# Kernel tuning notes

Measured on AMD Instinct MI355X. Metric: run time of the kernel, lower is better.

Reference implementation:

```python
import jax, jax.numpy as jnp
import numpy as np

EPS = 1e-07


def setup_inputs() -> dict:
    key = jax.random.key(0)
    k1, k2, k3, k4, k5, k6 = jax.random.split(key, 6)
    B, S, E = 128, 512, 64  # batch, seq_len == n_items, emb_size
    user_emb = jax.random.normal(k1, (B, S, E), dtype=jnp.float32)
    item_emb = jax.random.normal(k2, (B, S, E), dtype=jnp.float32)
    cluster_weights = jax.random.uniform(k3, (B, S, 1), dtype=jnp.float32)
    # binary keep-mask over sequence positions (multiplicative)
    last_item_mask = (jax.random.uniform(k4, (B, 1, S)) > 0.5).astype(jnp.float32)
    proj_w = jax.random.normal(k5, (1, 1), dtype=jnp.float32)
    proj_b = jax.random.normal(k6, (1,), dtype=jnp.float32)
    return {
        "user_emb": user_emb,
        "item_emb": item_emb,
        "cluster_weights": cluster_weights,
        "last_item_mask": last_item_mask,
        "proj_w": proj_w,
        "proj_b": proj_b,
    }


def reference(user_emb, item_emb, cluster_weights, last_item_mask, proj_w, proj_b):
    # L2-normalize with clamped norm (matches torch.clamp(norm, 1e-7))
    u = user_emb / jnp.maximum(jnp.linalg.norm(user_emb, axis=-1, keepdims=True), EPS)
    v = item_emb / jnp.maximum(jnp.linalg.norm(item_emb, axis=-1, keepdims=True), EPS)
    # cosine sim: [B, n_items, seq_len] (n_items == seq_len == S)
    cos = jnp.einsum("bse,bne->bns", u, v)
    # cluster_weights [B,S,1] broadcasts over the seq_len axis, indexed by dim1
    # (faithful to torch broadcast of [B,N,S,1] * [B,S,1,1] with N == S)
    sims = cos * cluster_weights  # [B,N,S]
    # Linear(1,1) + sigmoid applied elementwise (scalar affine)
    sims = jax.nn.sigmoid(sims * proj_w[0, 0] + proj_b[0])
    # permute to [B, seq_len, n_items], mask [B,1,S] broadcasts over last axis
    sims = jnp.swapaxes(sims, 1, 2) * last_item_mask
    # max over dim 2 -> [B, seq_len]
    return jnp.max(sims, axis=2)
```

## Files before the change

kernel.cpp:

```cpp
#include <hip/hip_runtime.h>
#include <hip/hip_bf16.h>
#include <math.h>

#define B_ 128
#define S_ 512
#define E_ 64
#define PAD_ 72

typedef short bf16x8 __attribute__((ext_vector_type(8)));
typedef float f32x4 __attribute__((ext_vector_type(4)));

__device__ __forceinline__ unsigned short f2b(float f) {
  __hip_bfloat16 h = __float2bfloat16(f);
  unsigned short u;
  __builtin_memcpy(&u, &h, 2);
  return u;
}

__device__ __forceinline__ void norm_store(const f32x4 x[4], float scl_num,
                                           unsigned short* dst) {
  float ss = 0.f;
#pragma unroll
  for (int i = 0; i < 4; ++i)
#pragma unroll
    for (int j = 0; j < 4; ++j) ss = fmaf(x[i][j], x[i][j], ss);
  ss += __shfl_xor(ss, 16);
  ss += __shfl_xor(ss, 32);
  float s = scl_num / fmaxf(sqrtf(ss), 1e-7f);
  bf16x8 o0, o1;
#pragma unroll
  for (int i = 0; i < 2; ++i)
#pragma unroll
    for (int j = 0; j < 4; ++j) {
      o0[i * 4 + j] = (short)f2b(x[i][j] * s);
      o1[i * 4 + j] = (short)f2b(x[i + 2][j] * s);
    }
  *(bf16x8*)dst = o0;
  *(bf16x8*)(dst + 8) = o1;
}

__global__ __launch_bounds__(1024) void fused_kernel(
    const float* __restrict__ ue, const float* __restrict__ ve,
    const float* __restrict__ cw, const float* __restrict__ mask,
    const float* __restrict__ pw, const float* __restrict__ pb,
    float* __restrict__ out) {
  __shared__ unsigned short vlds[S_ * PAD_];
  __shared__ unsigned short ulds[256 * PAD_];
  __shared__ float comb[4][256];

  const int bx = blockIdx.x;
  const int b = (bx & 7) * 16 + (bx >> 4);
  const int shalf = (bx >> 3) & 1;

  const int tid = threadIdx.x;
  const int wv = tid >> 6;
  const int lane = tid & 63;
  const int c = lane & 15;
  const int g = lane >> 4;
  const int ws = wv >> 2;
  const int wn = wv & 3;

  const float w0 = pw[0];
  const float* __restrict__ vb = ve + (size_t)b * S_ * E_;
  const float* __restrict__ cwb = cw + (size_t)b * S_;
  const float* __restrict__ ub = ue + ((size_t)b * S_ + shalf * 256) * E_;
  const float* __restrict__ mb = mask + (size_t)b * S_;

  const int vr0 = wv * 32 + c, vr1 = vr0 + 16, ur = wv * 16 + c;
  const f32x4* pv0 = (const f32x4*)(vb + (size_t)vr0 * E_ + g * 16);
  const f32x4* pv1 = (const f32x4*)(vb + (size_t)vr1 * E_ + g * 16);
  const f32x4* pu = (const f32x4*)(ub + (size_t)ur * E_ + g * 16);
  f32x4 xv0[4], xv1[4], xu[4];
#pragma unroll
  for (int i = 0; i < 4; ++i) {
    xv0[i] = pv0[i];
    xv1[i] = pv1[i];
    xu[i] = pu[i];
  }
  float cw0 = cwb[vr0] * w0;
  float cw1 = cwb[vr1] * w0;
  float pen[8];
#pragma unroll
  for (int j = 0; j < 8; ++j)
    pen[j] = (mb[(wn * 8 + j) * 16 + c] > 0.5f) ? 0.0f : -1e30f;

  norm_store(xv0, cw0, vlds + (size_t)vr0 * PAD_ + g * 16);
  norm_store(xv1, cw1, vlds + (size_t)vr1 * PAD_ + g * 16);
  norm_store(xu, 1.0f, ulds + (size_t)ur * PAD_ + g * 16);

  __syncthreads();

  const unsigned short* urp = ulds + (size_t)(ws * 64 + c) * PAD_ + g * 8;
  bf16x8 a[4][2];
#pragma unroll
  for (int st = 0; st < 4; ++st) {
    a[st][0] = *(const bf16x8*)(urp + st * 16 * PAD_);
    a[st][1] = *(const bf16x8*)(urp + st * 16 * PAD_ + 32);
  }

  float r[4][4];
#pragma unroll
  for (int st = 0; st < 4; ++st)
#pragma unroll
    for (int i = 0; i < 4; ++i) r[st][i] = -INFINITY;

#pragma unroll
  for (int j = 0; j < 8; ++j) {
    int it = wn * 8 + j;
    const unsigned short* vr = vlds + (size_t)(it * 16 + c) * PAD_ + g * 8;
    bf16x8 b0 = *(const bf16x8*)(vr);
    bf16x8 b1 = *(const bf16x8*)(vr + 32);
    f32x4 ci = {pen[j], pen[j], pen[j], pen[j]};
#pragma unroll
    for (int st = 0; st < 4; ++st) {
      f32x4 acc = __builtin_amdgcn_mfma_f32_16x16x32_bf16(a[st][0], b0, ci, 0, 0, 0);
      acc = __builtin_amdgcn_mfma_f32_16x16x32_bf16(a[st][1], b1, acc, 0, 0, 0);
      r[st][0] = fmaxf(r[st][0], acc[0]);
      r[st][1] = fmaxf(r[st][1], acc[1]);
      r[st][2] = fmaxf(r[st][2], acc[2]);
      r[st][3] = fmaxf(r[st][3], acc[3]);
    }
  }

#pragma unroll
  for (int st = 0; st < 4; ++st)
#pragma unroll
    for (int i = 0; i < 4; ++i) {
      float v = r[st][i];
      v = fmaxf(v, __shfl_xor(v, 1)); v = fmaxf(v, __shfl_xor(v, 2));
      v = fmaxf(v, __shfl_xor(v, 4)); v = fmaxf(v, __shfl_xor(v, 8));
      r[st][i] = v;
    }

  if (c == 0) {
#pragma unroll
    for (int st = 0; st < 4; ++st)
#pragma unroll
      for (int i = 0; i < 4; ++i)
        comb[wn][ws * 64 + st * 16 + g * 4 + i] = r[st][i];
  }

  __syncthreads();

  if (tid < 256) {
    float v = fmaxf(fmaxf(comb[0][tid], comb[1][tid]),
                    fmaxf(comb[2][tid], comb[3][tid]));
    float bias = pb[0];
    out[(size_t)b * S_ + shalf * 256 + tid] =
        (v < -1e29f) ? 0.0f : 1.0f / (1.0f + expf(-(v + bias)));
  }
}

extern "C" void kernel_launch(void* const* d_in, const int* in_sizes, int n_in,
                              void* d_out, int out_size, void* d_ws, size_t ws_size,
                              hipStream_t stream) {
  const float* ue = (const float*)d_in[0];
  const float* ve = (const float*)d_in[1];
  const float* cw = (const float*)d_in[2];
  const float* mask = (const float*)d_in[3];
  const float* pw = (const float*)d_in[4];
  const float* pb = (const float*)d_in[5];
  float* out = (float*)d_out;

  hipLaunchKernelGGL(fused_kernel, dim3(2 * B_), dim3(1024), 0, stream,
                     ue, ve, cw, mask, pw, pb, out);
}
```

Before: 19.13 us.

## Split each batch across four 512-thread blocks and normalize user rows in registers

The grid changes from 256 blocks of 1024 threads, each covering half of a batch's rows, to 512 blocks of 512 threads, each covering a quarter. User-embedding rows are now loaded in the layout the MFMA A operand needs, then normalized and converted to bf16 directly in registers, which removes the user LDS buffer and one round trip through shared memory. The aim is more resident blocks and better latency hiding, helped by launch bounds of 4 blocks per CU. The cost is that each batch's item embeddings are now normalized four times instead of twice, which adds global reads and redundant normalize work.

Result: slower. 27.90 us (+45.8%).

```diff
diff --git a/kernel.cpp b/kernel.cpp
--- a/kernel.cpp
+++ b/kernel.cpp
@@ -17,40 +17,17 @@
   return u;
 }
 
-__device__ __forceinline__ void norm_store(const f32x4 x[4], float scl_num,
-                                           unsigned short* dst) {
-  float ss = 0.f;
-#pragma unroll
-  for (int i = 0; i < 4; ++i)
-#pragma unroll
-    for (int j = 0; j < 4; ++j) ss = fmaf(x[i][j], x[i][j], ss);
-  ss += __shfl_xor(ss, 16);
-  ss += __shfl_xor(ss, 32);
-  float s = scl_num / fmaxf(sqrtf(ss), 1e-7f);
-  bf16x8 o0, o1;
-#pragma unroll
-  for (int i = 0; i < 2; ++i)
-#pragma unroll
-    for (int j = 0; j < 4; ++j) {
-      o0[i * 4 + j] = (short)f2b(x[i][j] * s);
-      o1[i * 4 + j] = (short)f2b(x[i + 2][j] * s);
-    }
-  *(bf16x8*)dst = o0;
-  *(bf16x8*)(dst + 8) = o1;
-}
-
-__global__ __launch_bounds__(1024) void fused_kernel(
+__global__ __launch_bounds__(512, 4) void fused_kernel(
     const float* __restrict__ ue, const float* __restrict__ ve,
     const float* __restrict__ cw, const float* __restrict__ mask,
     const float* __restrict__ pw, const float* __restrict__ pb,
     float* __restrict__ out) {
   __shared__ unsigned short vlds[S_ * PAD_];
-  __shared__ unsigned short ulds[256 * PAD_];
-  __shared__ float comb[4][256];
+  __shared__ float comb[4][128];
 
   const int bx = blockIdx.x;
-  const int b = (bx & 7) * 16 + (bx >> 4);
-  const int shalf = (bx >> 3) & 1;
+  const int b = (bx & 7) * 16 + (bx >> 5);
+  const int sq = (bx >> 3) & 3;
 
   const int tid = threadIdx.x;
   const int wv = tid >> 6;
@@ -63,40 +40,70 @@
   const float w0 = pw[0];
   const float* __restrict__ vb = ve + (size_t)b * S_ * E_;
   const float* __restrict__ cwb = cw + (size_t)b * S_;
-  const float* __restrict__ ub = ue + ((size_t)b * S_ + shalf * 256) * E_;
+  const float* __restrict__ ub = ue + ((size_t)b * S_ + sq * 128) * E_;
   const float* __restrict__ mb = mask + (size_t)b * S_;
 
-  const int vr0 = wv * 32 + c, vr1 = vr0 + 16, ur = wv * 16 + c;
-  const f32x4* pv0 = (const f32x4*)(vb + (size_t)vr0 * E_ + g * 16);
-  const f32x4* pv1 = (const f32x4*)(vb + (size_t)vr1 * E_ + g * 16);
-  const f32x4* pu = (const f32x4*)(ub + (size_t)ur * E_ + g * 16);
-  f32x4 xv0[4], xv1[4], xu[4];
+  f32x4 xu[4][4];
 #pragma unroll
-  for (int i = 0; i < 4; ++i) {
-    xv0[i] = pv0[i];
-    xv1[i] = pv1[i];
-    xu[i] = pu[i];
+  for (int st = 0; st < 4; ++st) {
+    const float* r = ub + (size_t)(ws * 64 + st * 16 + c) * E_;
+    xu[st][0] = *(const f32x4*)(r + 8 * g);
+    xu[st][1] = *(const f32x4*)(r + 8 * g + 4);
+    xu[st][2] = *(const f32x4*)(r + 8 * g + 32);
+    xu[st][3] = *(const f32x4*)(r + 8 * g + 36);
   }
-  float cw0 = cwb[vr0] * w0;
-  float cw1 = cwb[vr1] * w0;
   float pen[8];
 #pragma unroll
   for (int j = 0; j < 8; ++j)
     pen[j] = (mb[(wn * 8 + j) * 16 + c] > 0.5f) ? 0.0f : -1e30f;
 
-  norm_store(xv0, cw0, vlds + (size_t)vr0 * PAD_ + g * 16);
-  norm_store(xv1, cw1, vlds + (size_t)vr1 * PAD_ + g * 16);
-  norm_store(xu, 1.0f, ulds + (size_t)ur * PAD_ + g * 16);
+#pragma unroll
+  for (int q = 0; q < 4; ++q) {
+    const int row = wv * 64 + q * 16 + c;
+    const float* r = vb + (size_t)row * E_ + g * 16;
+    f32x4 x0 = *(const f32x4*)(r);
+    f32x4 x1 = *(const f32x4*)(r + 4);
+    f32x4 x2 = *(const f32x4*)(r + 8);
+    f32x4 x3 = *(const f32x4*)(r + 12);
+    float ss = 0.f;
+#pragma unroll
+    for (int j = 0; j < 4; ++j)
+      ss = fmaf(x0[j], x0[j], fmaf(x1[j], x1[j], fmaf(x2[j], x2[j], fmaf(x3[j], x3[j], ss))));
+    ss += __shfl_xor(ss, 16);
+    ss += __shfl_xor(ss, 32);
+    float s = (w0 * cwb[row]) / fmaxf(sqrtf(ss), 1e-7f);
+    bf16x8 o0, o1;
+#pragma unroll
+    for (int j = 0; j < 4; ++j) {
+      o0[j] = (short)f2b(x0[j] * s); o0[4 + j] = (short)f2b(x1[j] * s);
+      o1[j] = (short)f2b(x2[j] * s); o1[4 + j] = (short)f2b(x3[j] * s);
+    }
+    unsigned short* dst = vlds + (size_t)row * PAD_ + g * 16;
+    *(bf16x8*)dst = o0;
+    *(bf16x8*)(dst + 8) = o1;
+  }
 
-  __syncthreads();
-
-  const unsigned short* urp = ulds + (size_t)(ws * 64 + c) * PAD_ + g * 8;
   bf16x8 a[4][2];
 #pragma unroll
   for (int st = 0; st < 4; ++st) {
-    a[st][0] = *(const bf16x8*)(urp + st * 16 * PAD_);
-    a[st][1] = *(const bf16x8*)(urp + st * 16 * PAD_ + 32);
+    float ss = 0.f;
+#pragma unroll
+    for (int i = 0; i < 4; ++i)
+#pragma unroll
+      for (int j = 0; j < 4; ++j) ss = fmaf(xu[st][i][j], xu[st][i][j], ss);
+    ss += __shfl_xor(ss, 16);
+    ss += __shfl_xor(ss, 32);
+    float s = 1.0f / fmaxf(sqrtf(ss), 1e-7f);
+#pragma unroll
+    for (int j = 0; j < 4; ++j) {
+      a[st][0][j] = (short)f2b(xu[st][0][j] * s);
+      a[st][0][4 + j] = (short)f2b(xu[st][1][j] * s);
+      a[st][1][j] = (short)f2b(xu[st][2][j] * s);
+      a[st][1][4 + j] = (short)f2b(xu[st][3][j] * s);
+    }
   }
+
+  __syncthreads();
 
   float r[4][4];
 #pragma unroll
@@ -106,7 +113,7 @@
 
 #pragma unroll
   for (int j = 0; j < 8; ++j) {
-    int it = wn * 8 + j;
+    const int it = wn * 8 + j;
     const unsigned short* vr = vlds + (size_t)(it * 16 + c) * PAD_ + g * 8;
     bf16x8 b0 = *(const bf16x8*)(vr);
     bf16x8 b1 = *(const bf16x8*)(vr + 32);
@@ -142,11 +149,11 @@
 
   __syncthreads();
 
-  if (tid < 256) {
+  if (tid < 128) {
     float v = fmaxf(fmaxf(comb[0][tid], comb[1][tid]),
                     fmaxf(comb[2][tid], comb[3][tid]));
     float bias = pb[0];
-    out[(size_t)b * S_ + shalf * 256 + tid] =
+    out[(size_t)b * S_ + sq * 128 + tid] =
         (v < -1e29f) ? 0.0f : 1.0f / (1.0f + expf(-(v + bias)));
   }
 }
@@ -162,6 +169,6 @@
   const float* pb = (const float*)d_in[5];
   float* out = (float*)d_out;
 
-  hipLaunchKernelGGL(fused_kernel, dim3(2 * B_), dim3(1024), 0, stream,
+  hipLaunchKernelGGL(fused_kernel, dim3(4 * B_), dim3(512), 0, stream,
                      ue, ve, cw, mask, pw, pb, out);
 }
```

## Split item-embedding staging into two phases to overlap loads with MFMA

Applied to the files above, without the earlier changes.

The item embeddings are now staged in two halves. Each block first loads and normalizes the half matching its own user rows and runs MFMAs on it. The load of the other half is issued before that compute, and that half is normalized and stored after it, separated by an extra barrier. The aim is to hide part of the global load latency behind matrix work, at the cost of one more __syncthreads and holding the second half's registers live during the first compute phase.

Result: faster. 18.39 us (-3.9%).

```diff
diff --git a/kernel.cpp b/kernel.cpp
--- a/kernel.cpp
+++ b/kernel.cpp
@@ -15,28 +15,6 @@
   unsigned short u;
   __builtin_memcpy(&u, &h, 2);
   return u;
-}
-
-__device__ __forceinline__ void norm_store(const f32x4 x[4], float scl_num,
-                                           unsigned short* dst) {
-  float ss = 0.f;
-#pragma unroll
-  for (int i = 0; i < 4; ++i)
-#pragma unroll
-    for (int j = 0; j < 4; ++j) ss = fmaf(x[i][j], x[i][j], ss);
-  ss += __shfl_xor(ss, 16);
-  ss += __shfl_xor(ss, 32);
-  float s = scl_num / fmaxf(sqrtf(ss), 1e-7f);
-  bf16x8 o0, o1;
-#pragma unroll
-  for (int i = 0; i < 2; ++i)
-#pragma unroll
-    for (int j = 0; j < 4; ++j) {
-      o0[i * 4 + j] = (short)f2b(x[i][j] * s);
-      o1[i * 4 + j] = (short)f2b(x[i + 2][j] * s);
-    }
-  *(bf16x8*)dst = o0;
-  *(bf16x8*)(dst + 8) = o1;
 }
 
 __global__ __launch_bounds__(1024) void fused_kernel(
@@ -66,29 +44,72 @@
   const float* __restrict__ ub = ue + ((size_t)b * S_ + shalf * 256) * E_;
   const float* __restrict__ mb = mask + (size_t)b * S_;
 
-  const int vr0 = wv * 32 + c, vr1 = vr0 + 16, ur = wv * 16 + c;
-  const f32x4* pv0 = (const f32x4*)(vb + (size_t)vr0 * E_ + g * 16);
-  const f32x4* pv1 = (const f32x4*)(vb + (size_t)vr1 * E_ + g * 16);
-  const f32x4* pu = (const f32x4*)(ub + (size_t)ur * E_ + g * 16);
-  f32x4 xv0[4], xv1[4], xu[4];
-#pragma unroll
-  for (int i = 0; i < 4; ++i) {
-    xv0[i] = pv0[i];
-    xv1[i] = pv1[i];
-    xu[i] = pu[i];
-  }
-  float cw0 = cwb[vr0] * w0;
-  float cw1 = cwb[vr1] * w0;
+  const int vrow_own = shalf * 256 + wv * 16 + c;
+  const int vrow_oth = (1 - shalf) * 256 + wv * 16 + c;
+  const int urow = wv * 16 + c;
+
+  const float* pv = vb + (size_t)vrow_own * E_ + g * 16;
+  const float* pu = ub + (size_t)urow * E_ + g * 16;
+  f32x4 xv[4], xu[4];
+#pragma unroll
+  for (int i = 0; i < 4; ++i) xv[i] = ((const f32x4*)pv)[i];
+#pragma unroll
+  for (int i = 0; i < 4; ++i) xu[i] = ((const f32x4*)pu)[i];
+  float cwv = cwb[vrow_own];
   float pen[8];
 #pragma unroll
-  for (int j = 0; j < 8; ++j)
-    pen[j] = (mb[(wn * 8 + j) * 16 + c] > 0.5f) ? 0.0f : -1e30f;
-
-  norm_store(xv0, cw0, vlds + (size_t)vr0 * PAD_ + g * 16);
-  norm_store(xv1, cw1, vlds + (size_t)vr1 * PAD_ + g * 16);
-  norm_store(xu, 1.0f, ulds + (size_t)ur * PAD_ + g * 16);
+  for (int j = 0; j < 4; ++j) {
+    pen[j] = (mb[(shalf * 16 + wn * 4 + j) * 16 + c] > 0.5f) ? 0.0f : -1e30f;
+    pen[4 + j] =
+        (mb[((1 - shalf) * 16 + wn * 4 + j) * 16 + c] > 0.5f) ? 0.0f : -1e30f;
+  }
+
+  {
+    float ss = 0.f;
+#pragma unroll
+    for (int i = 0; i < 4; ++i)
+#pragma unroll
+      for (int j = 0; j < 4; ++j) ss = fmaf(xv[i][j], xv[i][j], ss);
+    ss += __shfl_xor(ss, 16);
+    ss += __shfl_xor(ss, 32);
+    float s = (w0 * cwv) / fmaxf(sqrtf(ss), 1e-7f);
+    bf16x8 o0, o1;
+#pragma unroll
+    for (int j = 0; j < 4; ++j) {
+      o0[j] = (short)f2b(xv[0][j] * s); o0[4 + j] = (short)f2b(xv[1][j] * s);
+      o1[j] = (short)f2b(xv[2][j] * s); o1[4 + j] = (short)f2b(xv[3][j] * s);
+    }
+    unsigned short* dst = vlds + (size_t)vrow_own * PAD_ + g * 16;
+    *(bf16x8*)dst = o0;
+    *(bf16x8*)(dst + 8) = o1;
+  }
+  {
+    float ss = 0.f;
+#pragma unroll
+    for (int i = 0; i < 4; ++i)
+#pragma unroll
+      for (int j = 0; j < 4; ++j) ss = fmaf(xu[i][j], xu[i][j], ss);
+    ss += __shfl_xor(ss, 16);
+    ss += __shfl_xor(ss, 32);
+    float s = 1.0f / fmaxf(sqrtf(ss), 1e-7f);
+    bf16x8 o0, o1;
+#pragma unroll
+    for (int j = 0; j < 4; ++j) {
+      o0[j] = (short)f2b(xu[0][j] * s); o0[4 + j] = (short)f2b(xu[1][j] * s);
+      o1[j] = (short)f2b(xu[2][j] * s); o1[4 + j] = (short)f2b(xu[3][j] * s);
+    }
+    unsigned short* dst = ulds + (size_t)urow * PAD_ + g * 16;
+    *(bf16x8*)dst = o0;
+    *(bf16x8*)(dst + 8) = o1;
+  }
 
   __syncthreads();
+
+  const float* py = vb + (size_t)vrow_oth * E_ + g * 16;
+  f32x4 yv[4];
+#pragma unroll
+  for (int i = 0; i < 4; ++i) yv[i] = ((const f32x4*)py)[i];
+  float cwo = cwb[vrow_oth];
 
   const unsigned short* urp = ulds + (size_t)(ws * 64 + c) * PAD_ + g * 8;
   bf16x8 a[4][2];
@@ -105,12 +126,52 @@
     for (int i = 0; i < 4; ++i) r[st][i] = -INFINITY;
 
 #pragma unroll
-  for (int j = 0; j < 8; ++j) {
-    int it = wn * 8 + j;
+  for (int j = 0; j < 4; ++j) {
+    const int it = shalf * 16 + wn * 4 + j;
     const unsigned short* vr = vlds + (size_t)(it * 16 + c) * PAD_ + g * 8;
     bf16x8 b0 = *(const bf16x8*)(vr);
     bf16x8 b1 = *(const bf16x8*)(vr + 32);
     f32x4 ci = {pen[j], pen[j], pen[j], pen[j]};
+#pragma unroll
+    for (int st = 0; st < 4; ++st) {
+      f32x4 acc = __builtin_amdgcn_mfma_f32_16x16x32_bf16(a[st][0], b0, ci, 0, 0, 0);
+      acc = __builtin_amdgcn_mfma_f32_16x16x32_bf16(a[st][1], b1, acc, 0, 0, 0);
+      r[st][0] = fmaxf(r[st][0], acc[0]);
+      r[st][1] = fmaxf(r[st][1], acc[1]);
+      r[st][2] = fmaxf(r[st][2], acc[2]);
+      r[st][3] = fmaxf(r[st][3], acc[3]);
+    }
+  }
+
+  {
+    float ss = 0.f;
+#pragma unroll
+    for (int i = 0; i < 4; ++i)
+#pragma unroll
+      for (int j = 0; j < 4; ++j) ss = fmaf(yv[i][j], yv[i][j], ss);
+    ss += __shfl_xor(ss, 16);
+    ss += __shfl_xor(ss, 32);
+    float s = (w0 * cwo) / fmaxf(sqrtf(ss), 1e-7f);
+    bf16x8 o0, o1;
+#pragma unroll
+    for (int j = 0; j < 4; ++j) {
+      o0[j] = (short)f2b(yv[0][j] * s); o0[4 + j] = (short)f2b(yv[1][j] * s);
+      o1[j] = (short)f2b(yv[2][j] * s); o1[4 + j] = (short)f2b(yv[3][j] * s);
+    }
+    unsigned short* dst = vlds + (size_t)vrow_oth * PAD_ + g * 16;
+    *(bf16x8*)dst = o0;
+    *(bf16x8*)(dst + 8) = o1;
+  }
+
+  __syncthreads();
+
+#pragma unroll
+  for (int j = 0; j < 4; ++j) {
+    const int it = (1 - shalf) * 16 + wn * 4 + j;
+    const unsigned short* vr = vlds + (size_t)(it * 16 + c) * PAD_ + g * 8;
+    bf16x8 b0 = *(const bf16x8*)(vr);
+    bf16x8 b1 = *(const bf16x8*)(vr + 32);
+    f32x4 ci = {pen[4 + j], pen[4 + j], pen[4 + j], pen[4 + j]};
 #pragma unroll
     for (int st = 0; st < 4; ++st) {
       f32x4 acc = __builtin_amdgcn_mfma_f32_16x16x32_bf16(a[st][0], b0, ci, 0, 0, 0);
```

## Coalesce embedding loads and overlap second-half V normalization with MFMA

Applied to the files above, without the earlier changes.

Rewrites the normalize-and-store step so each wave reads 16 contiguous rows with fully coalesced loads and reduces norms via 16-lane shuffles. The item rows are split into the block's own half, normalized before the first barrier, and the other half, whose global loads are issued before the first MFMA pass and normalized afterward. A second barrier then gates MFMA over the other half. This aims to hide global memory latency behind compute, at the cost of an extra __syncthreads and more live registers.

Measured after the change: 17.53 us, median of 2. -8.4%, faster.

```diff
diff --git a/kernel.cpp b/kernel.cpp
--- a/kernel.cpp
+++ b/kernel.cpp
@@ -17,26 +17,30 @@
   return u;
 }
 
-__device__ __forceinline__ void norm_store(const f32x4 x[4], float scl_num,
-                                           unsigned short* dst) {
-  float ss = 0.f;
+__device__ __forceinline__ void norm16_coalesced(
+    const float* __restrict__ src,
+    const float* __restrict__ scl,
+    float w0, int c, int g, int lane,
+    unsigned short* __restrict__ lds_base) {
+  f32x4 x[4];
+  float sn[4];
+#pragma unroll
+  for (int i = 0; i < 4; ++i) x[i] = *(const f32x4*)(src + i * 256 + lane * 4);
 #pragma unroll
   for (int i = 0; i < 4; ++i)
-#pragma unroll
-    for (int j = 0; j < 4; ++j) ss = fmaf(x[i][j], x[i][j], ss);
-  ss += __shfl_xor(ss, 16);
-  ss += __shfl_xor(ss, 32);
-  float s = scl_num / fmaxf(sqrtf(ss), 1e-7f);
-  bf16x8 o0, o1;
-#pragma unroll
-  for (int i = 0; i < 2; ++i)
-#pragma unroll
-    for (int j = 0; j < 4; ++j) {
-      o0[i * 4 + j] = (short)f2b(x[i][j] * s);
-      o1[i * 4 + j] = (short)f2b(x[i + 2][j] * s);
-    }
-  *(bf16x8*)dst = o0;
-  *(bf16x8*)(dst + 8) = o1;
+    sn[i] = scl ? scl[i * 4 + g] * w0 : 1.0f;
+#pragma unroll
+  for (int i = 0; i < 4; ++i) {
+    float ss = x[i][0] * x[i][0] + x[i][1] * x[i][1] +
+               x[i][2] * x[i][2] + x[i][3] * x[i][3];
+    ss += __shfl_xor(ss, 1); ss += __shfl_xor(ss, 2);
+    ss += __shfl_xor(ss, 4); ss += __shfl_xor(ss, 8);
+    float s = sn[i] / fmaxf(sqrtf(ss), 1e-7f);
+    ushort4 o;
+    o.x = f2b(x[i][0] * s); o.y = f2b(x[i][1] * s);
+    o.z = f2b(x[i][2] * s); o.w = f2b(x[i][3] * s);
+    *(ushort4*)(lds_base + (size_t)(i * 4 + g) * PAD_ + c * 4) = o;
+  }
 }
 
 __global__ __launch_bounds__(1024) void fused_kernel(
@@ -66,29 +70,32 @@
   const float* __restrict__ ub = ue + ((size_t)b * S_ + shalf * 256) * E_;
   const float* __restrict__ mb = mask + (size_t)b * S_;
 
-  const int vr0 = wv * 32 + c, vr1 = vr0 + 16, ur = wv * 16 + c;
-  const f32x4* pv0 = (const f32x4*)(vb + (size_t)vr0 * E_ + g * 16);
-  const f32x4* pv1 = (const f32x4*)(vb + (size_t)vr1 * E_ + g * 16);
-  const f32x4* pu = (const f32x4*)(ub + (size_t)ur * E_ + g * 16);
-  f32x4 xv0[4], xv1[4], xu[4];
-#pragma unroll
-  for (int i = 0; i < 4; ++i) {
-    xv0[i] = pv0[i];
-    xv1[i] = pv1[i];
-    xu[i] = pu[i];
-  }
-  float cw0 = cwb[vr0] * w0;
-  float cw1 = cwb[vr1] * w0;
+  const int vown = shalf * 256 + wv * 16;
+  const int voth = (1 - shalf) * 256 + wv * 16;
+  const int urow = wv * 16;
+
   float pen[8];
 #pragma unroll
-  for (int j = 0; j < 8; ++j)
-    pen[j] = (mb[(wn * 8 + j) * 16 + c] > 0.5f) ? 0.0f : -1e30f;
-
-  norm_store(xv0, cw0, vlds + (size_t)vr0 * PAD_ + g * 16);
-  norm_store(xv1, cw1, vlds + (size_t)vr1 * PAD_ + g * 16);
-  norm_store(xu, 1.0f, ulds + (size_t)ur * PAD_ + g * 16);
+  for (int j = 0; j < 4; ++j) {
+    pen[j] = (mb[(shalf * 16 + wn * 4 + j) * 16 + c] > 0.5f) ? 0.0f : -1e30f;
+    pen[4 + j] =
+        (mb[((1 - shalf) * 16 + wn * 4 + j) * 16 + c] > 0.5f) ? 0.0f : -1e30f;
+  }
+
+  norm16_coalesced(vb + (size_t)vown * E_, cwb + vown, w0, c, g, lane,
+                   vlds + (size_t)vown * PAD_);
+  norm16_coalesced(ub + (size_t)urow * E_, nullptr, 1.0f, c, g, lane,
+                   ulds + (size_t)urow * PAD_);
 
   __syncthreads();
+
+  const float* psrc = vb + (size_t)voth * E_;
+  f32x4 y[4];
+#pragma unroll
+  for (int i = 0; i < 4; ++i) y[i] = *(const f32x4*)(psrc + i * 256 + lane * 4);
+  float cwo[4];
+#pragma unroll
+  for (int i = 0; i < 4; ++i) cwo[i] = cwb[voth + i * 4 + g];
 
   const unsigned short* urp = ulds + (size_t)(ws * 64 + c) * PAD_ + g * 8;
   bf16x8 a[4][2];
@@ -105,12 +112,45 @@
     for (int i = 0; i < 4; ++i) r[st][i] = -INFINITY;
 
 #pragma unroll
-  for (int j = 0; j < 8; ++j) {
-    int it = wn * 8 + j;
+  for (int j = 0; j < 4; ++j) {
+    const int it = shalf * 16 + wn * 4 + j;
     const unsigned short* vr = vlds + (size_t)(it * 16 + c) * PAD_ + g * 8;
     bf16x8 b0 = *(const bf16x8*)(vr);
     bf16x8 b1 = *(const bf16x8*)(vr + 32);
     f32x4 ci = {pen[j], pen[j], pen[j], pen[j]};
+#pragma unroll
+    for (int st = 0; st < 4; ++st) {
+      f32x4 acc = __builtin_amdgcn_mfma_f32_16x16x32_bf16(a[st][0], b0, ci, 0, 0, 0);
+      acc = __builtin_amdgcn_mfma_f32_16x16x32_bf16(a[st][1], b1, acc, 0, 0, 0);
+      r[st][0] = fmaxf(r[st][0], acc[0]);
+      r[st][1] = fmaxf(r[st][1], acc[1]);
+      r[st][2] = fmaxf(r[st][2], acc[2]);
+      r[st][3] = fmaxf(r[st][3], acc[3]);
+    }
+  }
+
+#pragma unroll
+  for (int i = 0; i < 4; ++i) {
+    float ss = y[i][0] * y[i][0] + y[i][1] * y[i][1] +
+               y[i][2] * y[i][2] + y[i][3] * y[i][3];
+    ss += __shfl_xor(ss, 1); ss += __shfl_xor(ss, 2);
+    ss += __shfl_xor(ss, 4); ss += __shfl_xor(ss, 8);
+    float s = (w0 * cwo[i]) / fmaxf(sqrtf(ss), 1e-7f);
+    ushort4 o;
+    o.x = f2b(y[i][0] * s); o.y = f2b(y[i][1] * s);
+    o.z = f2b(y[i][2] * s); o.w = f2b(y[i][3] * s);
+    *(ushort4*)(vlds + (size_t)(voth + i * 4 + g) * PAD_ + c * 4) = o;
+  }
+
+  __syncthreads();
+
+#pragma unroll
+  for (int j = 0; j < 4; ++j) {
+    const int it = (1 - shalf) * 16 + wn * 4 + j;
+    const unsigned short* vr = vlds + (size_t)(it * 16 + c) * PAD_ + g * 8;
+    bf16x8 b0 = *(const bf16x8*)(vr);
+    bf16x8 b1 = *(const bf16x8*)(vr + 32);
+    f32x4 ci = {pen[4 + j], pen[4 + j], pen[4 + j], pen[4 + j]};
 #pragma unroll
     for (int st = 0; st < 4; ++st) {
       f32x4 acc = __builtin_amdgcn_mfma_f32_16x16x32_bf16(a[st][0], b0, ci, 0, 0, 0);
```
